# Optimization experiments

Hardware: AMD Instinct MI355X
Metric: run time of the kernel (lower is better)

Reference implementation:

```python
import jax, jax.numpy as jnp
import numpy as np

_D, _R = 1024, 4096


def flow_multinomial(n, p):
    """n: [...], p: [..., k] -> mean [..., k], cov [..., k, k]."""
    mean = n[..., None] * p  # [..., k]
    k = p.shape[-1]
    eye = jnp.eye(k, dtype=p.dtype)
    # diag(mean) - n * p p^T
    cov = mean[..., None] * eye - n[..., None, None] * (p[..., :, None] * p[..., None, :])
    return mean, cov


def mvn_logprob(x, mean, cov):
    """Batched MVN log-prob via Cholesky. x/mean: [..., k], cov: [..., k, k]."""
    k = x.shape[-1]
    L = jnp.linalg.cholesky(cov)
    diff = (x - mean)[..., None]  # [..., k, 1]
    z = jax.lax.linalg.triangular_solve(L, diff, left_side=True, lower=True)
    quad = jnp.sum(z[..., 0] ** 2, axis=-1)
    logdet = 2.0 * jnp.sum(jnp.log(jnp.diagonal(L, axis1=-2, axis2=-1)), axis=-1)
    return -0.5 * (k * jnp.log(2.0 * jnp.pi) + logdet + quad)


def setup_inputs() -> dict:
    D, R = _D, _R
    key = jax.random.key(0)
    ks = jax.random.split(key, 20)
    u = lambda k, shape, lo, hi: jax.random.uniform(k, shape, minval=lo, maxval=hi, dtype=jnp.float32)
    N = u(ks[0], (R,), 1e6, 2e6)
    S = N * u(ks[1], (D, R), 0.4, 0.7)
    E = N * u(ks[2], (D, R), 0.005, 0.02)
    I = N * u(ks[3], (D, R), 0.005, 0.02)
    T = N * u(ks[4], (D, R), 0.002, 0.01)
    # observed flows for each transition (any finite values are valid)
    S_E = S[:-1] * u(ks[5], (D - 1, R), 0.0, 0.02)
    E_I = E[:-1] * u(ks[6], (D - 1, R), 0.1, 0.4)
    I_T = I[:-1] * u(ks[7], (D - 1, R), 0.1, 0.3)
    I_U = I[:-1] * u(ks[8], (D - 1, R), 0.1, 0.3)
    T_R = T[:-1] * u(ks[9], (D - 1, R), 0.2, 0.5)
    T_D = T[:-1] * u(ks[10], (D - 1, R), 0.0, 0.05)
    adjacency = u(ks[11], (R, R), 0.0, 1.0)
    logit_decay_E = jax.random.normal(ks[12], (), dtype=jnp.float32)
    logit_decay_I = jax.random.normal(ks[13], (), dtype=jnp.float32)
    logit_decay_T = jax.random.normal(ks[14], (), dtype=jnp.float32)
    detection_rate = u(ks[15], (D, R), 0.05, 0.95)
    recovery_rate = u(ks[16], (D, R), 0.05, 0.95)
    contagion_I = u(ks[17], (D, R), 0.1, 2.0)
    return dict(S=S, E=E, I=I, T=T, N=N, S_E=S_E, E_I=E_I, I_T=I_T, I_U=I_U,
                T_R=T_R, T_D=T_D, adjacency=adjacency,
                logit_decay_E=logit_decay_E, logit_decay_I=logit_decay_I,
                logit_decay_T=logit_decay_T, detection_rate=detection_rate,
                recovery_rate=recovery_rate, contagion_I=contagion_I)


def reference(S, E, I, T, N, S_E, E_I, I_T, I_U, T_R, T_D, adjacency,
              logit_decay_E, logit_decay_I, logit_decay_T,
              detection_rate, recovery_rate, contagion_I):
    decay_E = jax.nn.sigmoid(logit_decay_E)
    decay_I = jax.nn.sigmoid(logit_decay_I)
    decay_T = jax.nn.sigmoid(logit_decay_T)

    # states at the start of each transition t = 0 .. D-2
    So, Eo, Io, To = S[:-1], E[:-1], I[:-1], T[:-1]  # [D-1, R]

    # prob_S_E, vectorized over transitions: A @ I_t for each t
    AI = jnp.einsum('rq,tq->tr', adjacency, Io)       # [D-1, R]
    AN = adjacency @ N                                 # [R]
    p_SE = -jnp.expm1(-(contagion_I[:-1] * AI) / AN)   # [D-1, R]

    # S -> E (1-dim MVN)
    mS, cS = flow_multinomial(So, p_SE[..., None])
    lpS = mvn_logprob(S_E[..., None], mS, cS)

    # E -> I (1-dim MVN)
    p_EI = jnp.broadcast_to(decay_E, p_SE.shape)
    mE, cE = flow_multinomial(Eo, p_EI[..., None])
    lpE = mvn_logprob(E_I[..., None], mE, cE)

    # I -> (T, U) (2-dim MVN)
    det = detection_rate[:-1]
    pI = jnp.stack([det * decay_I, (1.0 - det) * decay_I], axis=-1)  # [D-1, R, 2]
    mI, cI = flow_multinomial(Io, pI)
    lpI = mvn_logprob(jnp.stack([I_T, I_U], axis=-1), mI, cI)

    # T -> (R, D) (2-dim MVN)
    rec = recovery_rate[:-1]
    pT = jnp.stack([rec * decay_T, (1.0 - rec) * decay_T], axis=-1)
    mT, cT = flow_multinomial(To, pT)
    lpT = mvn_logprob(jnp.stack([T_R, T_D], axis=-1), mT, cT)

    # sum over transitions -> per-region total log prob [R]
    return jnp.sum(lpS + lpE + lpI + lpT, axis=0)
```

## Files before the change

kernel.cpp:

```cpp
#include <hip/hip_runtime.h>
#include <hip/hip_bf16.h>
#include <math.h>

typedef __attribute__((ext_vector_type(8))) short bf16x8;
typedef __attribute__((ext_vector_type(4))) float f32x4;
typedef unsigned int u32;

__device__ inline ushort f2bf(float x) {
  union { float f; unsigned u; } c; c.f = x;
  unsigned u = c.u;
  u += 0x7fffu + ((u >> 16) & 1u);
  return (ushort)(u >> 16);
}

__device__ __forceinline__ float rcpf(float x) { return __builtin_amdgcn_rcpf(x); }

__device__ __forceinline__ void gl_lds16(const ushort* g, ushort* l) {
  __builtin_amdgcn_global_load_lds(
      (const __attribute__((address_space(1))) u32*)g,
      (__attribute__((address_space(3))) u32*)l, 16, 0, 0);
}

__global__ __launch_bounds__(256) void conv_fused(const float* __restrict__ adj,
                                                  const float* __restrict__ Nv,
                                                  const float* __restrict__ I,
                                                  ushort* __restrict__ adjbf,
                                                  ushort* __restrict__ Ibf,
                                                  float* __restrict__ AN,
                                                  int R, int nI) {
  const int bx = blockIdx.x;
  const int tid = threadIdx.x;
  if (bx < R) {
    const int r = bx;
    const float* row = adj + (size_t)r * R;
    ushort* orow = adjbf + (size_t)r * R;
    float acc = 0.f;
    for (int q0 = tid * 4; q0 < R; q0 += 256 * 4) {
      float4 v = *(const float4*)(row + q0);
      float4 nv = *(const float4*)(Nv + q0);
      acc += v.x * nv.x + v.y * nv.y + v.z * nv.z + v.w * nv.w;
      ushort4 o;
      o.x = f2bf(v.x); o.y = f2bf(v.y); o.z = f2bf(v.z); o.w = f2bf(v.w);
      *(ushort4*)(orow + q0) = o;
    }
    #pragma unroll
    for (int off = 32; off > 0; off >>= 1) acc += __shfl_down(acc, off, 64);
    __shared__ float red[4];
    if ((tid & 63) == 0) red[tid >> 6] = acc;
    __syncthreads();
    if (tid == 0) AN[r] = red[0] + red[1] + red[2] + red[3];
  } else {
    int i = ((bx - R) * 256 + tid) * 4;
    if (i + 3 < nI) {
      float4 v = *(const float4*)(I + i);
      ushort4 o;
      o.x = f2bf(v.x); o.y = f2bf(v.y); o.z = f2bf(v.z); o.w = f2bf(v.w);
      *(ushort4*)(Ibf + i) = o;
    }
  }
}

__global__ __launch_bounds__(256) void gemm_bt_lds(const ushort* __restrict__ A,
                                                   const ushort* __restrict__ B,
                                                   float* __restrict__ C,
                                                   int M, int N, int K, int Ksplit) {
  __shared__ __align__(16) ushort sA[128 * 32];
  __shared__ __align__(16) ushort sB[128 * 32];
  const int tid = threadIdx.x;
  const int bn = blockIdx.x, bm = blockIdx.y, bz = blockIdx.z;
  const int wave = tid >> 6, lane = tid & 63;
  const int wm = (wave >> 1) * 64, wn = (wave & 1) * 64;

  const int p0 = wave * 2, p1 = wave * 2 + 1;
  const int lrow = lane >> 2;
  const int sblk = (lane & 3) ^ (lrow & 3);
  const int scol = sblk * 8;
  const size_t kbase = (size_t)bz * Ksplit + scol;
  const ushort* Ag0 = A + (size_t)(bm * 128 + p0 * 16 + lrow) * K + kbase;
  const ushort* Ag1 = A + (size_t)(bm * 128 + p1 * 16 + lrow) * K + kbase;
  const ushort* Bg0 = B + (size_t)(bn * 128 + p0 * 16 + lrow) * K + kbase;
  const ushort* Bg1 = B + (size_t)(bn * 128 + p1 * 16 + lrow) * K + kbase;
  ushort* sA0 = sA + p0 * 16 * 32;
  ushort* sA1 = sA + p1 * 16 * 32;
  ushort* sB0 = sB + p0 * 16 * 32;
  ushort* sB1 = sB + p1 * 16 * 32;

  const int fm = lane & 15;
  const int fkb = lane >> 4;
  const int pblk = (fkb ^ (fm & 3)) * 8;

  f32x4 acc[4][4];
  #pragma unroll
  for (int i = 0; i < 4; ++i)
    #pragma unroll
    for (int j = 0; j < 4; ++j) acc[i][j] = (f32x4){0.f, 0.f, 0.f, 0.f};

  for (int k0 = 0; k0 < Ksplit; k0 += 32) {
    __syncthreads();
    gl_lds16(Ag0 + k0, sA0);
    gl_lds16(Ag1 + k0, sA1);
    gl_lds16(Bg0 + k0, sB0);
    gl_lds16(Bg1 + k0, sB1);
    __syncthreads();
    bf16x8 af[4], bfr[4];
    #pragma unroll
    for (int i = 0; i < 4; ++i)
      af[i] = *(const bf16x8*)(sA + (wm + i * 16 + fm) * 32 + pblk);
    #pragma unroll
    for (int j = 0; j < 4; ++j)
      bfr[j] = *(const bf16x8*)(sB + (wn + j * 16 + fm) * 32 + pblk);
    #pragma unroll
    for (int i = 0; i < 4; ++i)
      #pragma unroll
      for (int j = 0; j < 4; ++j)
        acc[i][j] = __builtin_amdgcn_mfma_f32_16x16x32_bf16(af[i], bfr[j], acc[i][j], 0, 0, 0);
  }

  float* Cz = C + (size_t)bz * M * N;
  const int cm = (lane >> 4) * 4, cn = lane & 15;
  #pragma unroll
  for (int i = 0; i < 4; ++i)
    #pragma unroll
    for (int j = 0; j < 4; ++j) {
      size_t base = (size_t)(bm * 128 + wm + i * 16 + cm) * N + (bn * 128 + wn + j * 16 + cn);
      #pragma unroll
      for (int v = 0; v < 4; ++v)
        Cz[base + (size_t)v * N] = acc[i][j][v];
    }
}

__device__ __forceinline__ float elem_ll(float Sv, float Ev, float Iv, float Tv,
                                         float sev, float eiv, float itv, float iuv,
                                         float trv, float tdv, float dev, float rev,
                                         float cov, float aiv, float ran_,
                                         float dE, float omE, float dI, float omI,
                                         float dT, float omT) {
  float p = -expm1f(-(cov * aiv) * ran_);
  float mS = Sv * p;
  float varS = mS * (1.f - p);
  float dS = sev - mS;
  float mE = Ev * dE;
  float varE = mE * omE;
  float dEd = eiv - mE;
  float p1 = dev * dI, p2 = (1.f - dev) * dI;
  float d1 = itv - Iv * p1;
  float d2 = iuv - Iv * p2;
  float denI = Iv * p1 * p2 * omI;
  float qI = (d1 * d1 * p2 * (1.f - p2) + 2.f * d1 * d2 * p1 * p2 +
              d2 * d2 * p1 * (1.f - p1)) * rcpf(denI);
  float q1 = rev * dT, q2 = (1.f - rev) * dT;
  float e1 = trv - Tv * q1;
  float e2 = tdv - Tv * q2;
  float denT = Tv * q1 * q2 * omT;
  float qT = (e1 * e1 * q2 * (1.f - q2) + 2.f * e1 * e2 * q1 * q2 +
              e2 * e2 * q1 * (1.f - q1)) * rcpf(denT);

  float quad = dS * dS * rcpf(varS) + dEd * dEd * rcpf(varE) + qI + qT;
  float lg = __logf((varS * varE) * ((Iv * denI) * (Tv * denT)));
  return lg + quad;
}

template <int NS>
__global__ __launch_bounds__(256, 4) void logprob_kernel(
    const float* __restrict__ S, const float* __restrict__ E,
    const float* __restrict__ I, const float* __restrict__ T,
    const float* __restrict__ S_E, const float* __restrict__ E_I,
    const float* __restrict__ I_T, const float* __restrict__ I_U,
    const float* __restrict__ T_R, const float* __restrict__ T_D,
    const float* __restrict__ detr, const float* __restrict__ recr,
    const float* __restrict__ cont, const float* __restrict__ AI,
    const float* __restrict__ AN,
    const float* __restrict__ pldE, const float* __restrict__ pldI,
    const float* __restrict__ pldT, float* __restrict__ partial, int D1, int R) {
  const int r0 = (blockIdx.x * 256 + threadIdx.x) * 4;
  const size_t sstride = (size_t)(D1 + 1) * R;
  const float dE = 1.f / (1.f + __expf(-pldE[0]));
  const float dI = 1.f / (1.f + __expf(-pldI[0]));
  const float dT = 1.f / (1.f + __expf(-pldT[0]));
  const float omE = 1.f - dE, omI = 1.f - dI, omT = 1.f - dT;
  const float L2PI = 1.8378770664093453f;
  float4 an4 = *(const float4*)(AN + r0);
  float ran_[4] = {rcpf(an4.x), rcpf(an4.y), rcpf(an4.z), rcpf(an4.w)};

  const int t0 = blockIdx.y * 2;
  const bool two = (t0 + 1 < D1);
  const float wB = two ? 1.f : 0.f;
  const size_t iA = (size_t)t0 * R + r0;
  const size_t iB = iA + (two ? (size_t)R : 0);

#define LD4(arr, i) (*(const float4*)((arr) + (i)))
  float4 SvA = LD4(S, iA),   SvB = LD4(S, iB);
  float4 EvA = LD4(E, iA),   EvB = LD4(E, iB);
  float4 IvA = LD4(I, iA),   IvB = LD4(I, iB);
  float4 TvA = LD4(T, iA),   TvB = LD4(T, iB);
  float4 seA = LD4(S_E, iA), seB = LD4(S_E, iB);
  float4 eiA = LD4(E_I, iA), eiB = LD4(E_I, iB);
  float4 itA = LD4(I_T, iA), itB = LD4(I_T, iB);
  float4 iuA = LD4(I_U, iA), iuB = LD4(I_U, iB);
  float4 trA = LD4(T_R, iA), trB = LD4(T_R, iB);
  float4 tdA = LD4(T_D, iA), tdB = LD4(T_D, iB);
  float4 deA = LD4(detr, iA), deB = LD4(detr, iB);
  float4 reA = LD4(recr, iA), reB = LD4(recr, iB);
  float4 coA = LD4(cont, iA), coB = LD4(cont, iB);

  float aiA[4] = {0.f, 0.f, 0.f, 0.f};
  float aiB[4] = {0.f, 0.f, 0.f, 0.f};
  #pragma unroll
  for (int s = 0; s < NS; ++s) {
    float4 a = LD4(AI, s * sstride + iA);
    float4 b = LD4(AI, s * sstride + iB);
    aiA[0] += a.x; aiA[1] += a.y; aiA[2] += a.z; aiA[3] += a.w;
    aiB[0] += b.x; aiB[1] += b.y; aiB[2] += b.z; aiB[3] += b.w;
  }
#undef LD4

  float accA[4], accB[4];
  {
    float Sa[4] = {SvA.x, SvA.y, SvA.z, SvA.w}, Ea[4] = {EvA.x, EvA.y, EvA.z, EvA.w};
    float Ia[4] = {IvA.x, IvA.y, IvA.z, IvA.w}, Ta[4] = {TvA.x, TvA.y, TvA.z, TvA.w};
    float sea[4] = {seA.x, seA.y, seA.z, seA.w}, eia[4] = {eiA.x, eiA.y, eiA.z, eiA.w};
    float ita[4] = {itA.x, itA.y, itA.z, itA.w}, iua[4] = {iuA.x, iuA.y, iuA.z, iuA.w};
    float tra[4] = {trA.x, trA.y, trA.z, trA.w}, tda[4] = {tdA.x, tdA.y, tdA.z, tdA.w};
    float dea[4] = {deA.x, deA.y, deA.z, deA.w}, rea[4] = {reA.x, reA.y, reA.z, reA.w};
    float coa[4] = {coA.x, coA.y, coA.z, coA.w};
    #pragma unroll
    for (int v = 0; v < 4; ++v)
      accA[v] = elem_ll(Sa[v], Ea[v], Ia[v], Ta[v], sea[v], eia[v], ita[v], iua[v],
                        tra[v], tda[v], dea[v], rea[v], coa[v], aiA[v], ran_[v],
                        dE, omE, dI, omI, dT, omT);
  }
  {
    float Sa[4] = {SvB.x, SvB.y, SvB.z, SvB.w}, Ea[4] = {EvB.x, EvB.y, EvB.z, EvB.w};
    float Ia[4] = {IvB.x, IvB.y, IvB.z, IvB.w}, Ta[4] = {TvB.x, TvB.y, TvB.z, TvB.w};
    float sea[4] = {seB.x, seB.y, seB.z, seB.w}, eia[4] = {eiB.x, eiB.y, eiB.z, eiB.w};
    float ita[4] = {itB.x, itB.y, itB.z, itB.w}, iua[4] = {iuB.x, iuB.y, iuB.z, iuB.w};
    float tra[4] = {trB.x, trB.y, trB.z, trB.w}, tda[4] = {tdB.x, tdB.y, tdB.z, tdB.w};
    float dea[4] = {deB.x, deB.y, deB.z, deB.w}, rea[4] = {reB.x, reB.y, reB.z, reB.w};
    float coa[4] = {coB.x, coB.y, coB.z, coB.w};
    #pragma unroll
    for (int v = 0; v < 4; ++v)
      accB[v] = elem_ll(Sa[v], Ea[v], Ia[v], Ta[v], sea[v], eia[v], ita[v], iua[v],
                        tra[v], tda[v], dea[v], rea[v], coa[v], aiB[v], ran_[v],
                        dE, omE, dI, omI, dT, omT);
  }

  const float cterm = -3.f * L2PI * (two ? 2.f : 1.f);
  float4 res;
  res.x = -0.5f * (accA[0] + wB * accB[0]) + cterm;
  res.y = -0.5f * (accA[1] + wB * accB[1]) + cterm;
  res.z = -0.5f * (accA[2] + wB * accB[2]) + cterm;
  res.w = -0.5f * (accA[3] + wB * accB[3]) + cterm;
  *(float4*)(partial + (size_t)blockIdx.y * R + r0) = res;
}

__global__ __launch_bounds__(256) void reduce_kernel(const float* __restrict__ part,
                                                     float* __restrict__ out,
                                                     int R, int NBY) {
  __shared__ float red[256];
  const int tid = threadIdx.x;
  const int r = blockIdx.x * 32 + (tid & 31);
  const int slice = tid >> 5;
  const int rows = NBY >> 3;
  float acc = 0.f;
  for (int k = 0; k < rows; ++k)
    acc += part[(size_t)(slice * rows + k) * R + r];
  red[tid] = acc;
  __syncthreads();
  if (tid < 32) {
    float s = red[tid];
    #pragma unroll
    for (int sl = 1; sl < 8; ++sl) s += red[sl * 32 + tid];
    out[r] = s;
  }
}

extern "C" void kernel_launch(void* const* d_in, const int* in_sizes, int n_in,
                              void* d_out, int out_size, void* d_ws, size_t ws_size,
                              hipStream_t stream) {
  const float* S    = (const float*)d_in[0];
  const float* E    = (const float*)d_in[1];
  const float* I    = (const float*)d_in[2];
  const float* T    = (const float*)d_in[3];
  const float* Nv   = (const float*)d_in[4];
  const float* S_E  = (const float*)d_in[5];
  const float* E_I  = (const float*)d_in[6];
  const float* I_T  = (const float*)d_in[7];
  const float* I_U  = (const float*)d_in[8];
  const float* T_R  = (const float*)d_in[9];
  const float* T_D  = (const float*)d_in[10];
  const float* adj  = (const float*)d_in[11];
  const float* ldE  = (const float*)d_in[12];
  const float* ldI  = (const float*)d_in[13];
  const float* ldT  = (const float*)d_in[14];
  const float* detr = (const float*)d_in[15];
  const float* recr = (const float*)d_in[16];
  const float* cont = (const float*)d_in[17];
  float* out = (float*)d_out;

  const int R  = in_sizes[4];
  const int D  = in_sizes[0] / R;
  const int D1 = D - 1;
  const int NBY = (D1 + 1) / 2;

  char* ws = (char*)d_ws;
  ushort* adjbf = (ushort*)ws;
  ushort* Ibf   = (ushort*)(ws + (size_t)R * R * 2);
  float*  AIbuf = (float*)(ws + (size_t)R * R * 2 + (size_t)D * R * 2);
  const size_t tail = (size_t)R * 4 + (size_t)NBY * R * 4;
  const size_t need4 = (size_t)R * R * 2 + (size_t)D * R * 2 +
                       4 * (size_t)D * R * 4 + tail;
  const int NS = (ws_size >= need4) ? 4 : 2;
  float* ANbuf   = (float*)((char*)AIbuf + (size_t)NS * D * R * 4);
  float* partial = ANbuf + R;

  const int nI = D * R;
  const int convBlocks = R + nI / (256 * 4);
  hipLaunchKernelGGL(conv_fused, dim3(convBlocks), dim3(256), 0, stream,
                     adj, Nv, I, adjbf, Ibf, ANbuf, R, nI);
  hipLaunchKernelGGL(gemm_bt_lds, dim3(R / 128, D / 128, NS), dim3(256), 0, stream,
                     Ibf, adjbf, AIbuf, D, R, R, R / NS);
  if (NS == 4) {
    hipLaunchKernelGGL(logprob_kernel<4>, dim3(R / 1024, NBY), dim3(256), 0, stream,
                       S, E, I, T, S_E, E_I, I_T, I_U, T_R, T_D, detr, recr, cont,
                       AIbuf, ANbuf, ldE, ldI, ldT, partial, D1, R);
  } else {
    hipLaunchKernelGGL(logprob_kernel<2>, dim3(R / 1024, NBY), dim3(256), 0, stream,
                       S, E, I, T, S_E, E_I, I_T, I_U, T_R, T_D, detr, recr, cont,
                       AIbuf, ANbuf, ldE, ldI, ldT, partial, D1, R);
  }
  hipLaunchKernelGGL(reduce_kernel, dim3(R / 32), dim3(256), 0, stream,
                     partial, out, R, NBY);
}
```

Before: 365.6 us.

## Double-buffer LDS tiles in bf16 GEMM to overlap loads with MFMA

Shared-memory tiles for A and B in the GEMM become two ping-pong buffers. The next K-slice is issued with async global-to-LDS loads while MFMAs run on the current buffer, leaving one barrier per iteration instead of two. The goal is to hide global load latency behind compute. The cost is doubled LDS use per block, which may reduce occupancy.

```diff
diff --git a/kernel.cpp b/kernel.cpp
--- a/kernel.cpp
+++ b/kernel.cpp
@@ -64,8 +64,8 @@
                                                    const ushort* __restrict__ B,
                                                    float* __restrict__ C,
                                                    int M, int N, int K, int Ksplit) {
-  __shared__ __align__(16) ushort sA[128 * 32];
-  __shared__ __align__(16) ushort sB[128 * 32];
+  __shared__ __align__(16) ushort sA[2][128 * 32];
+  __shared__ __align__(16) ushort sB[2][128 * 32];
   const int tid = threadIdx.x;
   const int bn = blockIdx.x, bm = blockIdx.y, bz = blockIdx.z;
   const int wave = tid >> 6, lane = tid & 63;
@@ -80,10 +80,8 @@
   const ushort* Ag1 = A + (size_t)(bm * 128 + p1 * 16 + lrow) * K + kbase;
   const ushort* Bg0 = B + (size_t)(bn * 128 + p0 * 16 + lrow) * K + kbase;
   const ushort* Bg1 = B + (size_t)(bn * 128 + p1 * 16 + lrow) * K + kbase;
-  ushort* sA0 = sA + p0 * 16 * 32;
-  ushort* sA1 = sA + p1 * 16 * 32;
-  ushort* sB0 = sB + p0 * 16 * 32;
-  ushort* sB1 = sB + p1 * 16 * 32;
+  const int lo0 = p0 * 16 * 32;
+  const int lo1 = p1 * 16 * 32;
 
   const int fm = lane & 15;
   const int fkb = lane >> 4;
@@ -95,26 +93,37 @@
     #pragma unroll
     for (int j = 0; j < 4; ++j) acc[i][j] = (f32x4){0.f, 0.f, 0.f, 0.f};
 
-  for (int k0 = 0; k0 < Ksplit; k0 += 32) {
-    __syncthreads();
-    gl_lds16(Ag0 + k0, sA0);
-    gl_lds16(Ag1 + k0, sA1);
-    gl_lds16(Bg0 + k0, sB0);
-    gl_lds16(Bg1 + k0, sB1);
-    __syncthreads();
+  auto STAGE = [&](int b, int k0) {
+    gl_lds16(Ag0 + k0, sA[b] + lo0);
+    gl_lds16(Ag1 + k0, sA[b] + lo1);
+    gl_lds16(Bg0 + k0, sB[b] + lo0);
+    gl_lds16(Bg1 + k0, sB[b] + lo1);
+  };
+  auto COMPUTE = [&](int b) {
     bf16x8 af[4], bfr[4];
     #pragma unroll
     for (int i = 0; i < 4; ++i)
-      af[i] = *(const bf16x8*)(sA + (wm + i * 16 + fm) * 32 + pblk);
+      af[i] = *(const bf16x8*)(sA[b] + (wm + i * 16 + fm) * 32 + pblk);
     #pragma unroll
     for (int j = 0; j < 4; ++j)
-      bfr[j] = *(const bf16x8*)(sB + (wn + j * 16 + fm) * 32 + pblk);
+      bfr[j] = *(const bf16x8*)(sB[b] + (wn + j * 16 + fm) * 32 + pblk);
     #pragma unroll
     for (int i = 0; i < 4; ++i)
       #pragma unroll
       for (int j = 0; j < 4; ++j)
         acc[i][j] = __builtin_amdgcn_mfma_f32_16x16x32_bf16(af[i], bfr[j], acc[i][j], 0, 0, 0);
-  }
+  };
+
+  STAGE(0, 0);
+  __syncthreads();
+  int cur = 0;
+  for (int k0 = 0; k0 + 32 < Ksplit; k0 += 32) {
+    STAGE(cur ^ 1, k0 + 32);
+    COMPUTE(cur);
+    __syncthreads();
+    cur ^= 1;
+  }
+  COMPUTE(cur);
 
   float* Cz = C + (size_t)bz * M * N;
   const int cm = (lane >> 4) * 4, cn = lane & 15;
```

New measurement: 355.3 us. -2.8%, faster.
